# Kernel optimization log

Hardware: AMD Instinct MI355X
Metric: run time of the kernel (lower is better)

The kernel has to match this reference:

```python
import jax, jax.numpy as jnp
import numpy as np


def setup_inputs() -> dict:
    key = jax.random.key(0)
    k1, k2 = jax.random.split(key)
    B, T, D = 8, 2048, 2048
    layer_in = jax.random.normal(k1, (B, T, D), dtype=jnp.float32)
    # nn.Linear(2D, 2D): weight [out=2D, in=2D], bias [2D]
    W_gate = jax.random.normal(k2, (2 * D, 2 * D), dtype=jnp.float32) * 0.02
    b_gate = jnp.zeros((2 * D,), dtype=jnp.float32)
    return {"layer_in": layer_in, "W_gate": W_gate, "b_gate": b_gate}


def reference(layer_in, W_gate, b_gate):
    # Cumulative average: tril(ones)/row_index @ x  ==  cumsum(x)/[1..t]
    t = layer_in.shape[1]
    denom = jnp.arange(1, t + 1, dtype=layer_in.dtype)[:, None]  # (t, 1)
    average_out = jnp.cumsum(layer_in, axis=1) / denom  # (B, t, D)
    # Gating: Linear(2D -> 2D) on concat(x, avg), then chunk into two gates
    gating_in = jnp.concatenate([layer_in, average_out], axis=-1)  # (B, t, 2D)
    gates = jnp.einsum('btk,ok->bto', gating_in, W_gate) + b_gate  # (B, t, 2D)
    input_gate, forget_gate = jnp.split(gates, 2, axis=2)
    gating_out = (jax.nn.sigmoid(input_gate) * layer_in
                  + jax.nn.sigmoid(forget_gate) * average_out)
    return gating_out, average_out
```

## Files before the change

### kernel.cpp

```cpp
#include <hip/hip_runtime.h>
#include <hip/hip_bf16.h>


#define Bb 8
#define Tt 2048
#define Dd 2048
#define Mm (Bb * Tt)
#define Kk 4096
#define NTK 128
#define NC 32
#define CT 64

typedef __bf16 bf16x8 __attribute__((ext_vector_type(8)));
typedef float f32x4 __attribute__((ext_vector_type(4)));

__device__ __forceinline__ void gload16(const void* g, void* l) {
    __builtin_amdgcn_global_load_lds(
        (const __attribute__((address_space(1))) unsigned int*)g,
        (__attribute__((address_space(3))) unsigned int*)l, 16, 0, 0);
}

__global__ void wconv_kernel(const float* __restrict__ W,
                             unsigned short* __restrict__ Wb, long n) {
    long i = ((long)blockIdx.x * blockDim.x + threadIdx.x) * 4;
    long stride = (long)gridDim.x * blockDim.x * 4;
    for (; i < n; i += stride) {
        float4 v = *(const float4*)(W + i);
        __hip_bfloat16 a = __float2bfloat16(v.x);
        __hip_bfloat16 b = __float2bfloat16(v.y);
        __hip_bfloat16 c = __float2bfloat16(v.z);
        __hip_bfloat16 d = __float2bfloat16(v.w);
        ushort4 u;
        u.x = *(unsigned short*)&a; u.y = *(unsigned short*)&b;
        u.z = *(unsigned short*)&c; u.w = *(unsigned short*)&d;
        *(ushort4*)(Wb + i) = u;
    }
}

__global__ void ksum_kernel(const float* __restrict__ X, float* __restrict__ S) {
    int d = blockIdx.y * 256 + threadIdx.x;
    int bc = blockIdx.x;
    int b = bc >> 5, c = bc & 31;
    const float* p = X + ((long)(b * Tt + c * CT)) * Dd + d;
    float s = 0.f;
#pragma unroll 8
    for (int t = 0; t < CT; ++t) s += p[(long)t * Dd];
    S[(long)bc * Dd + d] = s;
}

__global__ void kscan_kernel(const float* __restrict__ X, const float* __restrict__ S,
                             float* __restrict__ AVG, unsigned short* __restrict__ Gin) {
    int d = blockIdx.y * 256 + threadIdx.x;
    int bc = blockIdx.x;
    int b = bc >> 5, c = bc & 31;
    const float* Sp = S + (long)(b * NC) * Dd + d;
    float run = 0.f;
    for (int cc = 0; cc < c; ++cc) run += Sp[(long)cc * Dd];
    const float* p = X + ((long)(b * Tt + c * CT)) * Dd + d;
    long row = (long)b * Tt + c * CT;
    for (int tt = 0; tt < CT; ++tt) {
        float x = p[(long)tt * Dd];
        run += x;
        float av = run / (float)(c * CT + tt + 1);
        long r = row + tt;
        AVG[r * Dd + d] = av;
        __hip_bfloat16 xb = __float2bfloat16(x);
        __hip_bfloat16 ab = __float2bfloat16(av);
        Gin[r * 4096 + d] = *(unsigned short*)&xb;
        Gin[r * 4096 + 2048 + d] = *(unsigned short*)&ab;
    }
}

#define MFMA(va, vb, c_) c_ = __builtin_amdgcn_mfma_f32_16x16x32_bf16(va, vb, c_, 0, 0, 0)
#define DS(p_, i_) (*(const bf16x8*)((p_) + (i_) * 1024))

#define TILE_BODY(t_, DO_ISSUE)                                                   \
  {                                                                               \
    const int buf_ = (t_) & 3;                                                    \
    const char* pa = rA + buf_ * 32768;                                           \
    const char* pb = rB + buf_ * 32768;                                           \
    bf16x8 a0 = DS(pa,0), a1 = DS(pa,1), a2 = DS(pa,2), a3 = DS(pa,3);            \
    bf16x8 b0 = DS(pb,0), b1 = DS(pb,1), b2 = DS(pb,2), b3 = DS(pb,3);            \
    if (DO_ISSUE) {                                                               \
      char* nd = ldsb + (((t_) + 3) & 3) * 32768 + woff;                          \
      const long ko = ((long)(t_) + 3) * 64;                                      \
      gload16(gA0 + ko, nd);                                                      \
      gload16(gA1 + ko, nd + 8192);                                               \
    }                                                                             \
    __builtin_amdgcn_s_setprio(1);                                                \
    MFMA(a0,b0,acc[0][0]); MFMA(a0,b1,acc[0][1]); MFMA(a0,b2,acc[0][2]); MFMA(a0,b3,acc[0][3]); \
    MFMA(a1,b0,acc[1][0]); MFMA(a1,b1,acc[1][1]); MFMA(a1,b2,acc[1][2]); MFMA(a1,b3,acc[1][3]); \
    MFMA(a2,b0,acc[2][0]); MFMA(a2,b1,acc[2][1]); MFMA(a2,b2,acc[2][2]); MFMA(a2,b3,acc[2][3]); \
    MFMA(a3,b0,acc[3][0]); MFMA(a3,b1,acc[3][1]); MFMA(a3,b2,acc[3][2]); MFMA(a3,b3,acc[3][3]); \
    __builtin_amdgcn_s_setprio(0);                                                \
    bf16x8 a4 = DS(pa,4), a5 = DS(pa,5), a6 = DS(pa,6), a7 = DS(pa,7);            \
    if (DO_ISSUE) {                                                               \
      char* nd = ldsb + (((t_) + 3) & 3) * 32768 + 16384 + woff;                  \
      const long ko = ((long)(t_) + 3) * 64;                                      \
      gload16(gB0 + ko, nd);                                                      \
      gload16(gB1 + ko, nd + 8192);                                               \
    }                                                                             \
    __builtin_amdgcn_s_setprio(1);                                                \
    MFMA(a4,b0,acc[4][0]); MFMA(a4,b1,acc[4][1]); MFMA(a4,b2,acc[4][2]); MFMA(a4,b3,acc[4][3]); \
    MFMA(a5,b0,acc[5][0]); MFMA(a5,b1,acc[5][1]); MFMA(a5,b2,acc[5][2]); MFMA(a5,b3,acc[5][3]); \
    MFMA(a6,b0,acc[6][0]); MFMA(a6,b1,acc[6][1]); MFMA(a6,b2,acc[6][2]); MFMA(a6,b3,acc[6][3]); \
    MFMA(a7,b0,acc[7][0]); MFMA(a7,b1,acc[7][1]); MFMA(a7,b2,acc[7][2]); MFMA(a7,b3,acc[7][3]); \
    __builtin_amdgcn_s_setprio(0);                                                \
  }

#define BOUNDARY(N_)                                                              \
  asm volatile("s_waitcnt vmcnt(" #N_ ")" ::: "memory");                          \
  __builtin_amdgcn_s_barrier();                                                   \
  __builtin_amdgcn_sched_barrier(0);

__global__ __launch_bounds__(512, 2) void gemm8_kernel(
    const unsigned short* __restrict__ Gin,
    const unsigned short* __restrict__ Wb,
    const float* __restrict__ bias,
    const float* __restrict__ X,
    const float* __restrict__ AVG,
    float* __restrict__ OUT)
{
    __shared__ char lds[131072];
    char* ldsb = (char*)lds;

    const int tid = threadIdx.x;
    const int w = tid >> 6, l = tid & 63;
    const int wm = w >> 2, wn = w & 3;
    const int lm = l & 15;
    const int woff = w * 1024;

    const int bid = blockIdx.x;
    const int swz = (bid & 7) * 128 + (bid >> 3);
    const long m0 = (long)(swz & 63) * 256;
    const int n0 = (swz >> 6) * 128;

    const int srow = tid >> 2;
    const int schunk = (tid & 3) ^ ((tid >> 3) & 3);
    const char* gA0 = (const char*)Gin + (m0 + srow) * 8192 + schunk * 16;
    const char* gA1 = gA0 + 128 * 8192;
    const long jr0 = n0 + ((srow >> 6) << 5) + (srow & 31) + (((srow >> 5) & 1) << 11);
    const int j1 = 128 + srow;
    const long jr1 = n0 + ((j1 >> 6) << 5) + (j1 & 31) + (((j1 >> 5) & 1) << 11);
    const char* gB0 = (const char*)Wb + jr0 * 8192 + schunk * 16;
    const char* gB1 = (const char*)Wb + jr1 * 8192 + schunk * 16;

    const int cbyte = (((l >> 4) ^ ((lm >> 1) & 3))) * 16;
    const char* rA = ldsb + (wm * 128 + lm) * 64 + cbyte;
    const char* rB = ldsb + 16384 + (wn * 64 + lm) * 64 + cbyte;

    f32x4 acc[8][4] = {};

    {
        gload16(gA0,       ldsb + woff);
        gload16(gA1,       ldsb + 8192 + woff);
        gload16(gB0,       ldsb + 16384 + woff);
        gload16(gB1,       ldsb + 24576 + woff);
        gload16(gA0 + 64,  ldsb + 32768 + woff);
        gload16(gA1 + 64,  ldsb + 32768 + 8192 + woff);
        gload16(gB0 + 64,  ldsb + 32768 + 16384 + woff);
        gload16(gB1 + 64,  ldsb + 32768 + 24576 + woff);
        gload16(gA0 + 128, ldsb + 65536 + woff);
        gload16(gA1 + 128, ldsb + 65536 + 8192 + woff);
        gload16(gB0 + 128, ldsb + 65536 + 16384 + woff);
        gload16(gB1 + 128, ldsb + 65536 + 24576 + woff);
    }
    BOUNDARY(8);

#pragma unroll 1
    for (int t = 0; t < NTK - 3; ++t) {
        TILE_BODY(t, 1);
        BOUNDARY(8);
    }
    TILE_BODY(125, 0);
    BOUNDARY(4);
    TILE_BODY(126, 0);
    BOUNDARY(0);
    TILE_BODY(127, 0);

#pragma unroll
    for (int mi = 0; mi < 8; ++mi) {
        long rbase = m0 + wm * 128 + mi * 16 + (l >> 4) * 4;
#pragma unroll
        for (int nj = 0; nj < 2; ++nj) {
            int d = n0 + wn * 32 + nj * 16 + lm;
            float bi_ = bias[d];
            float bf_ = bias[d + 2048];
#pragma unroll
            for (int r = 0; r < 4; ++r) {
                long idx = (rbase + r) * 2048 + d;
                float gi = acc[mi][nj][r] + bi_;
                float gf = acc[mi][nj + 2][r] + bf_;
                float x = X[idx];
                float av = AVG[idx];
                float si = 1.f / (1.f + __expf(-gi));
                float sf = 1.f / (1.f + __expf(-gf));
                OUT[idx] = si * x + sf * av;
            }
        }
    }
}

extern "C" void kernel_launch(void* const* d_in, const int* in_sizes, int n_in,
                              void* d_out, int out_size, void* d_ws, size_t ws_size,
                              hipStream_t stream) {
    const float* X = (const float*)d_in[0];
    const float* W = (const float*)d_in[1];
    const float* bias = (const float*)d_in[2];

    float* OUT = (float*)d_out;
    float* AVG = OUT + (long)Mm * Dd;

    char* ws = (char*)d_ws;
    unsigned short* Wb  = (unsigned short*)ws;
    unsigned short* Gin = (unsigned short*)(ws + 33554432);
    float* S = (float*)(ws + 33554432 + 134217728);

    wconv_kernel<<<2048, 256, 0, stream>>>(W, Wb, (long)Kk * Kk);
    ksum_kernel<<<dim3(Bb * NC, Dd / 256), 256, 0, stream>>>(X, S);
    kscan_kernel<<<dim3(Bb * NC, Dd / 256), 256, 0, stream>>>(X, S, AVG, Gin);
    gemm8_kernel<<<1024, 512, 0, stream>>>(Gin, Wb, bias, X, AVG, OUT);
}
```

Measured before the change: 690.2 us.

## Switch GEMM to 32x32x16 MFMA with two-phase K split and XCD-aware tile mapping

Replaces the 16x16x32 bf16 MFMA inner loop with 32x32x16 MFMA instructions, splitting each 64-wide K tile into two phases that use swizzled LDS read offsets. This cuts LDS read count per FLOP and holds fewer, larger accumulators. The block-to-tile mapping is also reworked so that blocks on the same XCD share N tiles within a batch, which is meant to improve L2 reuse. An extra barrier per phase and a new epilogue row mapping come with the change.

```diff
diff --git a/kernel.cpp b/kernel.cpp
--- a/kernel.cpp
+++ b/kernel.cpp
@@ -12,7 +12,7 @@
 #define CT 64
 
 typedef __bf16 bf16x8 __attribute__((ext_vector_type(8)));
-typedef float f32x4 __attribute__((ext_vector_type(4)));
+typedef float f32x16 __attribute__((ext_vector_type(16)));
 
 __device__ __forceinline__ void gload16(const void* g, void* l) {
     __builtin_amdgcn_global_load_lds(
@@ -71,49 +71,39 @@
     }
 }
 
-#define MFMA(va, vb, c_) c_ = __builtin_amdgcn_mfma_f32_16x16x32_bf16(va, vb, c_, 0, 0, 0)
-#define DS(p_, i_) (*(const bf16x8*)((p_) + (i_) * 1024))
-
-#define TILE_BODY(t_, DO_ISSUE)                                                   \
-  {                                                                               \
-    const int buf_ = (t_) & 3;                                                    \
-    const char* pa = rA + buf_ * 32768;                                           \
-    const char* pb = rB + buf_ * 32768;                                           \
-    bf16x8 a0 = DS(pa,0), a1 = DS(pa,1), a2 = DS(pa,2), a3 = DS(pa,3);            \
-    bf16x8 b0 = DS(pb,0), b1 = DS(pb,1), b2 = DS(pb,2), b3 = DS(pb,3);            \
-    if (DO_ISSUE) {                                                               \
-      char* nd = ldsb + (((t_) + 3) & 3) * 32768 + woff;                          \
-      const long ko = ((long)(t_) + 3) * 64;                                      \
-      gload16(gA0 + ko, nd);                                                      \
-      gload16(gA1 + ko, nd + 8192);                                               \
-    }                                                                             \
-    __builtin_amdgcn_s_setprio(1);                                                \
-    MFMA(a0,b0,acc[0][0]); MFMA(a0,b1,acc[0][1]); MFMA(a0,b2,acc[0][2]); MFMA(a0,b3,acc[0][3]); \
-    MFMA(a1,b0,acc[1][0]); MFMA(a1,b1,acc[1][1]); MFMA(a1,b2,acc[1][2]); MFMA(a1,b3,acc[1][3]); \
-    MFMA(a2,b0,acc[2][0]); MFMA(a2,b1,acc[2][1]); MFMA(a2,b2,acc[2][2]); MFMA(a2,b3,acc[2][3]); \
-    MFMA(a3,b0,acc[3][0]); MFMA(a3,b1,acc[3][1]); MFMA(a3,b2,acc[3][2]); MFMA(a3,b3,acc[3][3]); \
-    __builtin_amdgcn_s_setprio(0);                                                \
-    bf16x8 a4 = DS(pa,4), a5 = DS(pa,5), a6 = DS(pa,6), a7 = DS(pa,7);            \
-    if (DO_ISSUE) {                                                               \
-      char* nd = ldsb + (((t_) + 3) & 3) * 32768 + 16384 + woff;                  \
-      const long ko = ((long)(t_) + 3) * 64;                                      \
-      gload16(gB0 + ko, nd);                                                      \
-      gload16(gB1 + ko, nd + 8192);                                               \
-    }                                                                             \
-    __builtin_amdgcn_s_setprio(1);                                                \
-    MFMA(a4,b0,acc[4][0]); MFMA(a4,b1,acc[4][1]); MFMA(a4,b2,acc[4][2]); MFMA(a4,b3,acc[4][3]); \
-    MFMA(a5,b0,acc[5][0]); MFMA(a5,b1,acc[5][1]); MFMA(a5,b2,acc[5][2]); MFMA(a5,b3,acc[5][3]); \
-    MFMA(a6,b0,acc[6][0]); MFMA(a6,b1,acc[6][1]); MFMA(a6,b2,acc[6][2]); MFMA(a6,b3,acc[6][3]); \
-    MFMA(a7,b0,acc[7][0]); MFMA(a7,b1,acc[7][1]); MFMA(a7,b2,acc[7][2]); MFMA(a7,b3,acc[7][3]); \
-    __builtin_amdgcn_s_setprio(0);                                                \
+#define MFMA32(va, vb, c_) c_ = __builtin_amdgcn_mfma_f32_32x32x16_bf16(va, vb, c_, 0, 0, 0)
+#define RD(p_, i_) (*(const bf16x8*)((p_) + (i_) * 2048))
+
+#define PH(t_, kk_, IA_, IB_)                                                   \
+  {                                                                             \
+    const int buf_ = (t_) & 3;                                                  \
+    const char* pa_ = ((kk_) ? rA1 : rA0) + buf_ * 32768;                       \
+    const char* pb_ = ((kk_) ? rB1 : rB0) + buf_ * 32768;                       \
+    bf16x8 a0 = RD(pa_,0), a1 = RD(pa_,1), a2 = RD(pa_,2), a3 = RD(pa_,3);      \
+    bf16x8 b0 = RD(pb_,0), b1 = RD(pb_,1);                                      \
+    if (IA_) { char* nd_ = ldsb + (((t_)+3)&3)*32768 + woff;                    \
+      const long ko_ = ((long)(t_)+3)*64;                                       \
+      gload16(gA0 + ko_, nd_); gload16(gA1 + ko_, nd_ + 8192); }                \
+    if (IB_) { char* nd_ = ldsb + (((t_)+3)&3)*32768 + 16384 + woff;            \
+      const long ko_ = ((long)(t_)+3)*64;                                       \
+      gload16(gB0 + ko_, nd_); gload16(gB1 + ko_, nd_ + 8192); }                \
+    __builtin_amdgcn_s_barrier();                                               \
+    __builtin_amdgcn_sched_barrier(0);                                          \
+    __builtin_amdgcn_s_setprio(1);                                              \
+    MFMA32(a0, b0, acc[0][0]); MFMA32(a0, b1, acc[0][1]);                       \
+    MFMA32(a1, b0, acc[1][0]); MFMA32(a1, b1, acc[1][1]);                       \
+    MFMA32(a2, b0, acc[2][0]); MFMA32(a2, b1, acc[2][1]);                       \
+    MFMA32(a3, b0, acc[3][0]); MFMA32(a3, b1, acc[3][1]);                       \
+    __builtin_amdgcn_s_setprio(0);                                              \
+    __builtin_amdgcn_sched_barrier(0);                                          \
   }
 
-#define BOUNDARY(N_)                                                              \
-  asm volatile("s_waitcnt vmcnt(" #N_ ")" ::: "memory");                          \
-  __builtin_amdgcn_s_barrier();                                                   \
+#define BOUNDARY(N_)                                                            \
+  asm volatile("s_waitcnt vmcnt(" #N_ ")" ::: "memory");                        \
+  __builtin_amdgcn_s_barrier();                                                 \
   __builtin_amdgcn_sched_barrier(0);
 
-__global__ __launch_bounds__(512, 2) void gemm8_kernel(
+__global__ __launch_bounds__(512, 2) void gemm32_kernel(
     const unsigned short* __restrict__ Gin,
     const unsigned short* __restrict__ Wb,
     const float* __restrict__ bias,
@@ -121,19 +111,25 @@
     const float* __restrict__ AVG,
     float* __restrict__ OUT)
 {
-    __shared__ char lds[131072];
+    __shared__ __attribute__((aligned(128))) char lds[131072];
     char* ldsb = (char*)lds;
 
     const int tid = threadIdx.x;
     const int w = tid >> 6, l = tid & 63;
     const int wm = w >> 2, wn = w & 3;
-    const int lm = l & 15;
+    const int la = l & 31;
+    const int lk = l >> 5;
     const int woff = w * 1024;
 
     const int bid = blockIdx.x;
-    const int swz = (bid & 7) * 128 + (bid >> 3);
-    const long m0 = (long)(swz & 63) * 256;
-    const int n0 = (swz >> 6) * 128;
+    const int batch = bid >> 8;
+    const int rr = bid & 255;
+    const int xcd = rr & 7;
+    const int j = rr >> 3;
+    const int nt = xcd * 2 + (j >> 4);
+    const int mt = batch * 16 + (j & 15);
+    const long m0 = (long)mt * 256;
+    const int n0 = nt * 128;
 
     const int srow = tid >> 2;
     const int schunk = (tid & 3) ^ ((tid >> 3) & 3);
@@ -145,11 +141,14 @@
     const char* gB0 = (const char*)Wb + jr0 * 8192 + schunk * 16;
     const char* gB1 = (const char*)Wb + jr1 * 8192 + schunk * 16;
 
-    const int cbyte = (((l >> 4) ^ ((lm >> 1) & 3))) * 16;
-    const char* rA = ldsb + (wm * 128 + lm) * 64 + cbyte;
-    const char* rB = ldsb + 16384 + (wn * 64 + lm) * 64 + cbyte;
-
-    f32x4 acc[8][4] = {};
+    const int cb0 = ((lk ^ ((la >> 1) & 3))) * 16;
+    const int cb1 = cb0 ^ 32;
+    const char* rA0 = ldsb + (wm * 128 + la) * 64 + cb0;
+    const char* rA1 = ldsb + (wm * 128 + la) * 64 + cb1;
+    const char* rB0 = ldsb + 16384 + (wn * 64 + la) * 64 + cb0;
+    const char* rB1 = ldsb + 16384 + (wn * 64 + la) * 64 + cb1;
+
+    f32x16 acc[4][2] = {};
 
     {
         gload16(gA0,       ldsb + woff);
@@ -169,34 +168,35 @@
 
 #pragma unroll 1
     for (int t = 0; t < NTK - 3; ++t) {
-        TILE_BODY(t, 1);
+        PH(t, 0, 1, 0);
+        PH(t, 1, 0, 1);
         BOUNDARY(8);
     }
-    TILE_BODY(125, 0);
+    PH(125, 0, 0, 0); PH(125, 1, 0, 0);
     BOUNDARY(4);
-    TILE_BODY(126, 0);
+    PH(126, 0, 0, 0); PH(126, 1, 0, 0);
     BOUNDARY(0);
-    TILE_BODY(127, 0);
-
+    PH(127, 0, 0, 0); PH(127, 1, 0, 0);
+
+    const int d = n0 + wn * 32 + la;
+    const float bi_ = bias[d];
+    const float bf_ = bias[d + 2048];
 #pragma unroll
-    for (int mi = 0; mi < 8; ++mi) {
-        long rbase = m0 + wm * 128 + mi * 16 + (l >> 4) * 4;
+    for (int mi = 0; mi < 4; ++mi) {
+        const long rb = m0 + wm * 128 + mi * 32 + lk * 4;
+        f32x16 ci = acc[mi][0];
+        f32x16 cf = acc[mi][1];
 #pragma unroll
-        for (int nj = 0; nj < 2; ++nj) {
-            int d = n0 + wn * 32 + nj * 16 + lm;
-            float bi_ = bias[d];
-            float bf_ = bias[d + 2048];
-#pragma unroll
-            for (int r = 0; r < 4; ++r) {
-                long idx = (rbase + r) * 2048 + d;
-                float gi = acc[mi][nj][r] + bi_;
-                float gf = acc[mi][nj + 2][r] + bf_;
-                float x = X[idx];
-                float av = AVG[idx];
-                float si = 1.f / (1.f + __expf(-gi));
-                float sf = 1.f / (1.f + __expf(-gf));
-                OUT[idx] = si * x + sf * av;
-            }
+        for (int q = 0; q < 16; ++q) {
+            long row = rb + (q & 3) + 8 * (q >> 2);
+            long idx = row * 2048 + d;
+            float gi = ci[q] + bi_;
+            float gf = cf[q] + bf_;
+            float x = X[idx];
+            float av = AVG[idx];
+            float si = 1.f / (1.f + __expf(-gi));
+            float sf = 1.f / (1.f + __expf(-gf));
+            OUT[idx] = si * x + sf * av;
         }
     }
 }
@@ -219,5 +219,5 @@
     wconv_kernel<<<2048, 256, 0, stream>>>(W, Wb, (long)Kk * Kk);
     ksum_kernel<<<dim3(Bb * NC, Dd / 256), 256, 0, stream>>>(X, S);
     kscan_kernel<<<dim3(Bb * NC, Dd / 256), 256, 0, stream>>>(X, S, AVG, Gin);
-    gemm8_kernel<<<1024, 512, 0, stream>>>(Gin, Wb, bias, X, AVG, OUT);
-}
+    gemm32_kernel<<<1024, 512, 0, stream>>>(Gin, Wb, bias, X, AVG, OUT);
+}
```

New measurement: 690.0 us. No clear change (-0.0%).

## Restructure GEMM into double-buffered ping-pong pipeline with register prefetch and bf16 epilogue

Applied to the files above, without the earlier changes.

Replaces the 4-stage LDS ring of the GEMM with a 2-buffer scheme (64KB LDS). Each tile is split into four MFMA quadrants separated by barriers, and LDS reads for the next tile are rotated through three register sets so reads overlap compute. The block-to-tile mapping is changed to group work by batch and XCD for L2 locality. The epilogue reads x and avg from the bf16 Gin buffer instead of the fp32 X/AVG arrays, which cuts epilogue traffic but loses precision in the output combine. The extra barriers per tile add synchronisation overhead.

```diff
diff --git a/kernel.cpp b/kernel.cpp
--- a/kernel.cpp
+++ b/kernel.cpp
@@ -7,7 +7,6 @@
 #define Dd 2048
 #define Mm (Bb * Tt)
 #define Kk 4096
-#define NTK 128
 #define NC 32
 #define CT 64
 
@@ -72,56 +71,84 @@
 }
 
 #define MFMA(va, vb, c_) c_ = __builtin_amdgcn_mfma_f32_16x16x32_bf16(va, vb, c_, 0, 0, 0)
-#define DS(p_, i_) (*(const bf16x8*)((p_) + (i_) * 1024))
-
-#define TILE_BODY(t_, DO_ISSUE)                                                   \
-  {                                                                               \
-    const int buf_ = (t_) & 3;                                                    \
-    const char* pa = rA + buf_ * 32768;                                           \
-    const char* pb = rB + buf_ * 32768;                                           \
-    bf16x8 a0 = DS(pa,0), a1 = DS(pa,1), a2 = DS(pa,2), a3 = DS(pa,3);            \
-    bf16x8 b0 = DS(pb,0), b1 = DS(pb,1), b2 = DS(pb,2), b3 = DS(pb,3);            \
-    if (DO_ISSUE) {                                                               \
-      char* nd = ldsb + (((t_) + 3) & 3) * 32768 + woff;                          \
-      const long ko = ((long)(t_) + 3) * 64;                                      \
-      gload16(gA0 + ko, nd);                                                      \
-      gload16(gA1 + ko, nd + 8192);                                               \
-    }                                                                             \
-    __builtin_amdgcn_s_setprio(1);                                                \
-    MFMA(a0,b0,acc[0][0]); MFMA(a0,b1,acc[0][1]); MFMA(a0,b2,acc[0][2]); MFMA(a0,b3,acc[0][3]); \
-    MFMA(a1,b0,acc[1][0]); MFMA(a1,b1,acc[1][1]); MFMA(a1,b2,acc[1][2]); MFMA(a1,b3,acc[1][3]); \
-    MFMA(a2,b0,acc[2][0]); MFMA(a2,b1,acc[2][1]); MFMA(a2,b2,acc[2][2]); MFMA(a2,b3,acc[2][3]); \
-    MFMA(a3,b0,acc[3][0]); MFMA(a3,b1,acc[3][1]); MFMA(a3,b2,acc[3][2]); MFMA(a3,b3,acc[3][3]); \
-    __builtin_amdgcn_s_setprio(0);                                                \
-    bf16x8 a4 = DS(pa,4), a5 = DS(pa,5), a6 = DS(pa,6), a7 = DS(pa,7);            \
-    if (DO_ISSUE) {                                                               \
-      char* nd = ldsb + (((t_) + 3) & 3) * 32768 + 16384 + woff;                  \
-      const long ko = ((long)(t_) + 3) * 64;                                      \
-      gload16(gB0 + ko, nd);                                                      \
-      gload16(gB1 + ko, nd + 8192);                                               \
-    }                                                                             \
-    __builtin_amdgcn_s_setprio(1);                                                \
-    MFMA(a4,b0,acc[4][0]); MFMA(a4,b1,acc[4][1]); MFMA(a4,b2,acc[4][2]); MFMA(a4,b3,acc[4][3]); \
-    MFMA(a5,b0,acc[5][0]); MFMA(a5,b1,acc[5][1]); MFMA(a5,b2,acc[5][2]); MFMA(a5,b3,acc[5][3]); \
-    MFMA(a6,b0,acc[6][0]); MFMA(a6,b1,acc[6][1]); MFMA(a6,b2,acc[6][2]); MFMA(a6,b3,acc[6][3]); \
-    MFMA(a7,b0,acc[7][0]); MFMA(a7,b1,acc[7][1]); MFMA(a7,b2,acc[7][2]); MFMA(a7,b3,acc[7][3]); \
-    __builtin_amdgcn_s_setprio(0);                                                \
+
+#define RDSET_RG0(S_, obb_)                                               \
+  a##S_##0 = *(const bf16x8*)(rA0 + (obb_));                              \
+  a##S_##1 = *(const bf16x8*)(rA0 + (obb_) + 1024);                       \
+  a##S_##2 = *(const bf16x8*)(rA0 + (obb_) + 2048);                       \
+  a##S_##3 = *(const bf16x8*)(rA0 + (obb_) + 3072);                       \
+  b##S_##0 = *(const bf16x8*)(rB0 + (obb_));                              \
+  b##S_##1 = *(const bf16x8*)(rB0 + (obb_) + 1024);
+
+#define RDSET_RG1(S_, obb_)                                               \
+  a##S_##0 = *(const bf16x8*)(rA0 + (obb_) + 4096);                       \
+  a##S_##1 = *(const bf16x8*)(rA0 + (obb_) + 5120);                       \
+  a##S_##2 = *(const bf16x8*)(rA0 + (obb_) + 6144);                       \
+  a##S_##3 = *(const bf16x8*)(rA0 + (obb_) + 7168);                       \
+  b##S_##0 = *(const bf16x8*)(rB0 + (obb_) + 2048);                       \
+  b##S_##1 = *(const bf16x8*)(rB0 + (obb_) + 3072);
+
+#define CL_M0(S_)                                                         \
+  MFMA(a##S_##0, b##S_##0, acc[0][0]); MFMA(a##S_##0, b##S_##1, acc[0][1]);\
+  MFMA(a##S_##1, b##S_##0, acc[1][0]); MFMA(a##S_##1, b##S_##1, acc[1][1]);\
+  MFMA(a##S_##2, b##S_##0, acc[2][0]); MFMA(a##S_##2, b##S_##1, acc[2][1]);\
+  MFMA(a##S_##3, b##S_##0, acc[3][0]); MFMA(a##S_##3, b##S_##1, acc[3][1]);
+#define CL_M1(SA_, SB_)                                                   \
+  MFMA(a##SA_##0, b##SB_##0, acc[0][2]); MFMA(a##SA_##0, b##SB_##1, acc[0][3]);\
+  MFMA(a##SA_##1, b##SB_##0, acc[1][2]); MFMA(a##SA_##1, b##SB_##1, acc[1][3]);\
+  MFMA(a##SA_##2, b##SB_##0, acc[2][2]); MFMA(a##SA_##2, b##SB_##1, acc[2][3]);\
+  MFMA(a##SA_##3, b##SB_##0, acc[3][2]); MFMA(a##SA_##3, b##SB_##1, acc[3][3]);
+#define CL_M2(SB_, SA_)                                                   \
+  MFMA(a##SB_##0, b##SA_##0, acc[4][0]); MFMA(a##SB_##0, b##SA_##1, acc[4][1]);\
+  MFMA(a##SB_##1, b##SA_##0, acc[5][0]); MFMA(a##SB_##1, b##SA_##1, acc[5][1]);\
+  MFMA(a##SB_##2, b##SA_##0, acc[6][0]); MFMA(a##SB_##2, b##SA_##1, acc[6][1]);\
+  MFMA(a##SB_##3, b##SA_##0, acc[7][0]); MFMA(a##SB_##3, b##SA_##1, acc[7][1]);
+#define CL_M3(SB_)                                                        \
+  MFMA(a##SB_##0, b##SB_##0, acc[4][2]); MFMA(a##SB_##0, b##SB_##1, acc[4][3]);\
+  MFMA(a##SB_##1, b##SB_##0, acc[5][2]); MFMA(a##SB_##1, b##SB_##1, acc[5][3]);\
+  MFMA(a##SB_##2, b##SB_##0, acc[6][2]); MFMA(a##SB_##2, b##SB_##1, acc[6][3]);\
+  MFMA(a##SB_##3, b##SB_##0, acc[7][2]); MFMA(a##SB_##3, b##SB_##1, acc[7][3]);
+
+#define SBAR __builtin_amdgcn_s_barrier()
+#define SCHB __builtin_amdgcn_sched_barrier(0)
+
+#define TILE(t_, bb_, CA_, CB_, NX_, STG_, VN_, RDS_)                     \
+  {                                                                       \
+                                   \
+    if (STG_) { const long ko_ = ((long)(t_) + 2) * 64;                   \
+      gload16(gA0 + ko_, ldsb + (bb_) + woff);                            \
+      gload16(gA1 + ko_, ldsb + (bb_) + 8192 + woff); }                   \
+    SCHB; SBAR; SCHB;                                                     \
+    __builtin_amdgcn_s_setprio(1); CL_M0(CA_); __builtin_amdgcn_s_setprio(0); \
+    SCHB; SBAR;                                                           \
+       \
+    if (STG_) { const long ko_ = ((long)(t_) + 2) * 64;                   \
+      gload16(gB0 + ko_, ldsb + (bb_) + 16384 + woff);                    \
+      gload16(gB1 + ko_, ldsb + (bb_) + 24576 + woff); }                  \
+    SCHB; SBAR; SCHB;                                                     \
+    __builtin_amdgcn_s_setprio(1); CL_M1(CA_, CB_); __builtin_amdgcn_s_setprio(0); \
+    SCHB;                                                                 \
+    asm volatile("s_waitcnt vmcnt(" #VN_ ")" ::: "memory");               \
+    SBAR;                                                                 \
+                               \
+    if (RDS_) { RDSET_RG0(NX_, (bb_) ^ 32768); }                          \
+    SCHB; SBAR; SCHB;                                                     \
+    __builtin_amdgcn_s_setprio(1); CL_M2(CB_, CA_); __builtin_amdgcn_s_setprio(0); \
+    SCHB; SBAR;                                                           \
+                                              \
+    if (RDS_) { RDSET_RG1(CA_, (bb_) ^ 32768); }                          \
+    SCHB; SBAR; SCHB;                                                     \
+    __builtin_amdgcn_s_setprio(1); CL_M3(CB_); __builtin_amdgcn_s_setprio(0); \
+    SCHB; SBAR;                                                           \
   }
 
-#define BOUNDARY(N_)                                                              \
-  asm volatile("s_waitcnt vmcnt(" #N_ ")" ::: "memory");                          \
-  __builtin_amdgcn_s_barrier();                                                   \
-  __builtin_amdgcn_sched_barrier(0);
-
-__global__ __launch_bounds__(512, 2) void gemm8_kernel(
+__global__ __launch_bounds__(512, 2) void gemm4p_kernel(
     const unsigned short* __restrict__ Gin,
     const unsigned short* __restrict__ Wb,
     const float* __restrict__ bias,
-    const float* __restrict__ X,
-    const float* __restrict__ AVG,
     float* __restrict__ OUT)
 {
-    __shared__ char lds[131072];
+    __shared__ __attribute__((aligned(128))) char lds[65536];
     char* ldsb = (char*)lds;
 
     const int tid = threadIdx.x;
@@ -131,9 +158,14 @@
     const int woff = w * 1024;
 
     const int bid = blockIdx.x;
-    const int swz = (bid & 7) * 128 + (bid >> 3);
-    const long m0 = (long)(swz & 63) * 256;
-    const int n0 = (swz >> 6) * 128;
+    const int batch = bid >> 8;
+    const int rr = bid & 255;
+    const int xcd = rr & 7;
+    const int j = rr >> 3;
+    const int nt = xcd * 2 + (j >> 4);
+    const int mt = batch * 16 + (j & 15);
+    const long m0 = (long)mt * 256;
+    const int n0 = nt * 128;
 
     const int srow = tid >> 2;
     const int schunk = (tid & 3) ^ ((tid >> 3) & 3);
@@ -146,37 +178,39 @@
     const char* gB1 = (const char*)Wb + jr1 * 8192 + schunk * 16;
 
     const int cbyte = (((l >> 4) ^ ((lm >> 1) & 3))) * 16;
-    const char* rA = ldsb + (wm * 128 + lm) * 64 + cbyte;
-    const char* rB = ldsb + 16384 + (wn * 64 + lm) * 64 + cbyte;
+    const char* rA0 = ldsb + (wm * 128 + lm) * 64 + cbyte;
+    const char* rB0 = ldsb + 16384 + (wn * 64 + lm) * 64 + cbyte;
 
     f32x4 acc[8][4] = {};
 
-    {
-        gload16(gA0,       ldsb + woff);
-        gload16(gA1,       ldsb + 8192 + woff);
-        gload16(gB0,       ldsb + 16384 + woff);
-        gload16(gB1,       ldsb + 24576 + woff);
-        gload16(gA0 + 64,  ldsb + 32768 + woff);
-        gload16(gA1 + 64,  ldsb + 32768 + 8192 + woff);
-        gload16(gB0 + 64,  ldsb + 32768 + 16384 + woff);
-        gload16(gB1 + 64,  ldsb + 32768 + 24576 + woff);
-        gload16(gA0 + 128, ldsb + 65536 + woff);
-        gload16(gA1 + 128, ldsb + 65536 + 8192 + woff);
-        gload16(gB0 + 128, ldsb + 65536 + 16384 + woff);
-        gload16(gB1 + 128, ldsb + 65536 + 24576 + woff);
-    }
-    BOUNDARY(8);
+    bf16x8 aA0{}, aA1{}, aA2{}, aA3{}, bA0{}, bA1{};
+    bf16x8 aB0{}, aB1{}, aB2{}, aB3{}, bB0{}, bB1{};
+    bf16x8 aC0{}, aC1{}, aC2{}, aC3{}, bC0{}, bC1{};
+
+    gload16(gA0,      ldsb + woff);
+    gload16(gA1,      ldsb + 8192 + woff);
+    gload16(gB0,      ldsb + 16384 + woff);
+    gload16(gB1,      ldsb + 24576 + woff);
+    gload16(gA0 + 64, ldsb + 32768 + woff);
+    gload16(gA1 + 64, ldsb + 32768 + 8192 + woff);
+    gload16(gB0 + 64, ldsb + 32768 + 16384 + woff);
+    gload16(gB1 + 64, ldsb + 32768 + 24576 + woff);
+    asm volatile("s_waitcnt vmcnt(4)" ::: "memory");
+    SBAR; SCHB;
+    RDSET_RG0(A, 0); RDSET_RG1(B, 0);
+    SCHB; SBAR;
 
 #pragma unroll 1
-    for (int t = 0; t < NTK - 3; ++t) {
-        TILE_BODY(t, 1);
-        BOUNDARY(8);
-    }
-    TILE_BODY(125, 0);
-    BOUNDARY(4);
-    TILE_BODY(126, 0);
-    BOUNDARY(0);
-    TILE_BODY(127, 0);
+    for (int t = 0; t < 126; t += 6) {
+        TILE(t + 0, 0,     A, B, C, 1, 4, 1)
+        TILE(t + 1, 32768, C, A, B, 1, 4, 1)
+        TILE(t + 2, 0,     B, C, A, 1, 4, 1)
+        TILE(t + 3, 32768, A, B, C, 1, 4, 1)
+        TILE(t + 4, 0,     C, A, B, 1, 4, 1)
+        TILE(t + 5, 32768, B, C, A, 1, 4, 1)
+    }
+    TILE(126, 0,     A, B, C, 0, 0, 1)
+    TILE(127, 32768, C, A, B, 0, 0, 0)
 
 #pragma unroll
     for (int mi = 0; mi < 8; ++mi) {
@@ -188,14 +222,16 @@
             float bf_ = bias[d + 2048];
 #pragma unroll
             for (int r = 0; r < 4; ++r) {
-                long idx = (rbase + r) * 2048 + d;
+                long row = rbase + r;
+                unsigned int ux = Gin[row * 4096 + d];
+                unsigned int ua = Gin[row * 4096 + 2048 + d];
+                union { unsigned int u; float f; } cx, ca;
+                cx.u = ux << 16; ca.u = ua << 16;
                 float gi = acc[mi][nj][r] + bi_;
                 float gf = acc[mi][nj + 2][r] + bf_;
-                float x = X[idx];
-                float av = AVG[idx];
                 float si = 1.f / (1.f + __expf(-gi));
                 float sf = 1.f / (1.f + __expf(-gf));
-                OUT[idx] = si * x + sf * av;
+                OUT[row * 2048 + d] = si * cx.f + sf * ca.f;
             }
         }
     }
@@ -219,5 +255,5 @@
     wconv_kernel<<<2048, 256, 0, stream>>>(W, Wb, (long)Kk * Kk);
     ksum_kernel<<<dim3(Bb * NC, Dd / 256), 256, 0, stream>>>(X, S);
     kscan_kernel<<<dim3(Bb * NC, Dd / 256), 256, 0, stream>>>(X, S, AVG, Gin);
-    gemm8_kernel<<<1024, 512, 0, stream>>>(Gin, Wb, bias, X, AVG, OUT);
-}
+    gemm4p_kernel<<<1024, 512, 0, stream>>>(Gin, Wb, bias, OUT);
+}
```

Measured after the change: 775.1 us. +12.3%, slower.

## Restructure GEMM main loop with barrier-split phases, new tile swizzle, bf16 epilogue reads

Applied to the files above, without the earlier changes.

Splits each K-tile into two barrier-separated phases, each with an explicit LDS-read wait before its MFMA burst. Remaps block IDs so tiles are grouped by batch and XCD, which should improve L2 locality for the weight tiles. The epilogue now reads x and avg as bf16 values from the staged gating input instead of fp32 from X and AVG, halving that traffic but reducing epilogue precision. The launch bound changes from two blocks per CU to one, which lets each thread use more registers.

```diff
diff --git a/kernel.cpp b/kernel.cpp
--- a/kernel.cpp
+++ b/kernel.cpp
@@ -7,7 +7,6 @@
 #define Dd 2048
 #define Mm (Bb * Tt)
 #define Kk 4096
-#define NTK 128
 #define NC 32
 #define CT 64
 
@@ -72,56 +71,55 @@
 }
 
 #define MFMA(va, vb, c_) c_ = __builtin_amdgcn_mfma_f32_16x16x32_bf16(va, vb, c_, 0, 0, 0)
-#define DS(p_, i_) (*(const bf16x8*)((p_) + (i_) * 1024))
-
-#define TILE_BODY(t_, DO_ISSUE)                                                   \
-  {                                                                               \
-    const int buf_ = (t_) & 3;                                                    \
-    const char* pa = rA + buf_ * 32768;                                           \
-    const char* pb = rB + buf_ * 32768;                                           \
-    bf16x8 a0 = DS(pa,0), a1 = DS(pa,1), a2 = DS(pa,2), a3 = DS(pa,3);            \
-    bf16x8 b0 = DS(pb,0), b1 = DS(pb,1), b2 = DS(pb,2), b3 = DS(pb,3);            \
-    if (DO_ISSUE) {                                                               \
-      char* nd = ldsb + (((t_) + 3) & 3) * 32768 + woff;                          \
-      const long ko = ((long)(t_) + 3) * 64;                                      \
-      gload16(gA0 + ko, nd);                                                      \
-      gload16(gA1 + ko, nd + 8192);                                               \
-    }                                                                             \
-    __builtin_amdgcn_s_setprio(1);                                                \
+#define RD(p_, i_) (*(const bf16x8*)((p_) + (i_) * 1024))
+#define SBAR __builtin_amdgcn_s_barrier()
+#define SCHB __builtin_amdgcn_sched_barrier(0)
+
+#define TILEBODY(t_, STG_)                                                      \
+  {                                                                             \
+    const int buf_ = (t_) & 3;                                                  \
+    const char* pa_ = rA0 + buf_ * 32768;                                       \
+    const char* pb_ = rB0 + buf_ * 32768;                                       \
+              \
+    bf16x8 a0 = RD(pa_,0), a1 = RD(pa_,1), a2 = RD(pa_,2), a3 = RD(pa_,3);      \
+    bf16x8 b0 = RD(pb_,0), b1 = RD(pb_,1), b2 = RD(pb_,2), b3 = RD(pb_,3);      \
+    if (STG_) { char* nd_ = ldsb + (((t_) + 3) & 3) * 32768 + woff;             \
+      const long ko_ = ((long)(t_) + 3) * 64;                                   \
+      gload16(gA0 + ko_, nd_); gload16(gA1 + ko_, nd_ + 8192); }                \
+    SCHB; SBAR;                                                                 \
+    asm volatile("s_waitcnt lgkmcnt(0)" ::: "memory"); SCHB;                    \
+    __builtin_amdgcn_s_setprio(1);                                              \
     MFMA(a0,b0,acc[0][0]); MFMA(a0,b1,acc[0][1]); MFMA(a0,b2,acc[0][2]); MFMA(a0,b3,acc[0][3]); \
     MFMA(a1,b0,acc[1][0]); MFMA(a1,b1,acc[1][1]); MFMA(a1,b2,acc[1][2]); MFMA(a1,b3,acc[1][3]); \
     MFMA(a2,b0,acc[2][0]); MFMA(a2,b1,acc[2][1]); MFMA(a2,b2,acc[2][2]); MFMA(a2,b3,acc[2][3]); \
     MFMA(a3,b0,acc[3][0]); MFMA(a3,b1,acc[3][1]); MFMA(a3,b2,acc[3][2]); MFMA(a3,b3,acc[3][3]); \
-    __builtin_amdgcn_s_setprio(0);                                                \
-    bf16x8 a4 = DS(pa,4), a5 = DS(pa,5), a6 = DS(pa,6), a7 = DS(pa,7);            \
-    if (DO_ISSUE) {                                                               \
-      char* nd = ldsb + (((t_) + 3) & 3) * 32768 + 16384 + woff;                  \
-      const long ko = ((long)(t_) + 3) * 64;                                      \
-      gload16(gB0 + ko, nd);                                                      \
-      gload16(gB1 + ko, nd + 8192);                                               \
-    }                                                                             \
-    __builtin_amdgcn_s_setprio(1);                                                \
+    __builtin_amdgcn_s_setprio(0); SCHB; SBAR;                                  \
+                   \
+    bf16x8 a4 = RD(pa_,4), a5 = RD(pa_,5), a6 = RD(pa_,6), a7 = RD(pa_,7);      \
+    if (STG_) { char* nd_ = ldsb + (((t_) + 3) & 3) * 32768 + 16384 + woff;     \
+      const long ko_ = ((long)(t_) + 3) * 64;                                   \
+      gload16(gB0 + ko_, nd_); gload16(gB1 + ko_, nd_ + 8192); }                \
+    SCHB; SBAR;                                                                 \
+    asm volatile("s_waitcnt lgkmcnt(0)" ::: "memory"); SCHB;                    \
+    __builtin_amdgcn_s_setprio(1);                                              \
     MFMA(a4,b0,acc[4][0]); MFMA(a4,b1,acc[4][1]); MFMA(a4,b2,acc[4][2]); MFMA(a4,b3,acc[4][3]); \
     MFMA(a5,b0,acc[5][0]); MFMA(a5,b1,acc[5][1]); MFMA(a5,b2,acc[5][2]); MFMA(a5,b3,acc[5][3]); \
     MFMA(a6,b0,acc[6][0]); MFMA(a6,b1,acc[6][1]); MFMA(a6,b2,acc[6][2]); MFMA(a6,b3,acc[6][3]); \
     MFMA(a7,b0,acc[7][0]); MFMA(a7,b1,acc[7][1]); MFMA(a7,b2,acc[7][2]); MFMA(a7,b3,acc[7][3]); \
-    __builtin_amdgcn_s_setprio(0);                                                \
+    __builtin_amdgcn_s_setprio(0); SCHB;                                        \
   }
 
-#define BOUNDARY(N_)                                                              \
-  asm volatile("s_waitcnt vmcnt(" #N_ ")" ::: "memory");                          \
-  __builtin_amdgcn_s_barrier();                                                   \
-  __builtin_amdgcn_sched_barrier(0);
-
-__global__ __launch_bounds__(512, 2) void gemm8_kernel(
+#define BOUNDARY(N_)                                                            \
+  asm volatile("s_waitcnt vmcnt(" #N_ ")" ::: "memory");                        \
+  SBAR; SCHB;
+
+__global__ __launch_bounds__(512, 1) void gemm2p_kernel(
     const unsigned short* __restrict__ Gin,
     const unsigned short* __restrict__ Wb,
     const float* __restrict__ bias,
-    const float* __restrict__ X,
-    const float* __restrict__ AVG,
     float* __restrict__ OUT)
 {
-    __shared__ char lds[131072];
+    __shared__ __attribute__((aligned(128))) char lds[131072];
     char* ldsb = (char*)lds;
 
     const int tid = threadIdx.x;
@@ -131,9 +129,14 @@
     const int woff = w * 1024;
 
     const int bid = blockIdx.x;
-    const int swz = (bid & 7) * 128 + (bid >> 3);
-    const long m0 = (long)(swz & 63) * 256;
-    const int n0 = (swz >> 6) * 128;
+    const int batch = bid >> 8;
+    const int rr = bid & 255;
+    const int xcd = rr & 7;
+    const int j = rr >> 3;
+    const int nt = xcd * 2 + (j >> 4);
+    const int mt = batch * 16 + (j & 15);
+    const long m0 = (long)mt * 256;
+    const int n0 = nt * 128;
 
     const int srow = tid >> 2;
     const int schunk = (tid & 3) ^ ((tid >> 3) & 3);
@@ -146,8 +149,8 @@
     const char* gB1 = (const char*)Wb + jr1 * 8192 + schunk * 16;
 
     const int cbyte = (((l >> 4) ^ ((lm >> 1) & 3))) * 16;
-    const char* rA = ldsb + (wm * 128 + lm) * 64 + cbyte;
-    const char* rB = ldsb + 16384 + (wn * 64 + lm) * 64 + cbyte;
+    const char* rA0 = ldsb + (wm * 128 + lm) * 64 + cbyte;
+    const char* rB0 = ldsb + 16384 + (wn * 64 + lm) * 64 + cbyte;
 
     f32x4 acc[8][4] = {};
 
@@ -168,15 +171,15 @@
     BOUNDARY(8);
 
 #pragma unroll 1
-    for (int t = 0; t < NTK - 3; ++t) {
-        TILE_BODY(t, 1);
+    for (int t = 0; t < 125; ++t) {
+        TILEBODY(t, 1);
         BOUNDARY(8);
     }
-    TILE_BODY(125, 0);
+    TILEBODY(125, 0);
     BOUNDARY(4);
-    TILE_BODY(126, 0);
+    TILEBODY(126, 0);
     BOUNDARY(0);
-    TILE_BODY(127, 0);
+    TILEBODY(127, 0);
 
 #pragma unroll
     for (int mi = 0; mi < 8; ++mi) {
@@ -188,14 +191,16 @@
             float bf_ = bias[d + 2048];
 #pragma unroll
             for (int r = 0; r < 4; ++r) {
-                long idx = (rbase + r) * 2048 + d;
+                long row = rbase + r;
+                unsigned int ux = Gin[row * 4096 + d];
+                unsigned int ua = Gin[row * 4096 + 2048 + d];
+                union { unsigned int u; float f; } cx, ca;
+                cx.u = ux << 16; ca.u = ua << 16;
                 float gi = acc[mi][nj][r] + bi_;
                 float gf = acc[mi][nj + 2][r] + bf_;
-                float x = X[idx];
-                float av = AVG[idx];
                 float si = 1.f / (1.f + __expf(-gi));
                 float sf = 1.f / (1.f + __expf(-gf));
-                OUT[idx] = si * x + sf * av;
+                OUT[row * 2048 + d] = si * cx.f + sf * ca.f;
             }
         }
     }
@@ -219,5 +224,5 @@
     wconv_kernel<<<2048, 256, 0, stream>>>(W, Wb, (long)Kk * Kk);
     ksum_kernel<<<dim3(Bb * NC, Dd / 256), 256, 0, stream>>>(X, S);
     kscan_kernel<<<dim3(Bb * NC, Dd / 256), 256, 0, stream>>>(X, S, AVG, Gin);
-    gemm8_kernel<<<1024, 512, 0, stream>>>(Gin, Wb, bias, X, AVG, OUT);
-}
+    gemm2p_kernel<<<1024, 512, 0, stream>>>(Gin, Wb, bias, OUT);
+}
```

After: 634.7 us. 1.09x faster.
